# Kernel optimization log

Measured on AMD Instinct MI355X. Metric: run time of the kernel, lower is better.

The kernel has to match this reference:

```python
import jax, jax.numpy as jnp
import numpy as np

DIM = 1024
HEADS = 16
HEAD_DIM = DIM // HEADS
SCALE = HEAD_DIM ** -0.5


def setup_inputs() -> dict:
    key = jax.random.key(0)
    ks = jax.random.split(key, 6)
    B, N, C = 2, 2048, DIM
    q = jax.random.normal(ks[0], (B, N, C), dtype=jnp.float32)
    k = jax.random.normal(ks[1], (B, N, C), dtype=jnp.float32)
    v = jax.random.normal(ks[2], (B, N, C), dtype=jnp.float32)
    # torch nn.Linear weights: out = x @ W.T (+ b); qkv has no bias (qkv_bias=False)
    W_qkv = jax.random.normal(ks[3], (3 * C, 3 * C), dtype=jnp.float32) * (3 * C) ** -0.5
    W_proj = jax.random.normal(ks[4], (C, C), dtype=jnp.float32) * C ** -0.5
    b_proj = jax.random.normal(ks[5], (C,), dtype=jnp.float32) * 0.02
    return {"q": q, "k": k, "v": v, "W_qkv": W_qkv, "W_proj": W_proj, "b_proj": b_proj}


def reference(q, k, v, W_qkv, W_proj, b_proj):
    B, N, C = q.shape
    # fused QKV projection on concatenated [q,k,v] -> [B,N,3C]
    qkv = jnp.concatenate([q, k, v], axis=-1) @ W_qkv.T
    qkv = qkv.reshape(B, N, 3, HEADS, HEAD_DIM).transpose(2, 0, 3, 1, 4)  # [3,B,H,N,hd]
    qh, kh, vh = qkv[0], qkv[1], qkv[2]
    attn = jnp.einsum('bhqd,bhkd->bhqk', qh, kh) * SCALE
    attn = jax.nn.softmax(attn, axis=-1)  # attn_drop is identity (p=0)
    x = jnp.einsum('bhqk,bhkd->bhqd', attn, vh)  # [B,H,N,hd]
    x = x.transpose(0, 2, 1, 3).reshape(B, N, C)
    x = x @ W_proj.T + b_proj  # proj_drop is identity (p=0)
    return x
```

## Files before the change

kernel.cpp:

```cpp
#include <hip/hip_runtime.h>
#include <hip/hip_bf16.h>
#include <stdint.h>

#define HEADS 16
#define HD 64
#define SEQ 2048
#define BATCH 2
#define CDIM 1024
#define MROWS (BATCH*SEQ)
#define K3C (3*CDIM)
#define QSCALE 0.1803368801111244f

typedef __bf16 bf16x8 __attribute__((ext_vector_type(8)));
typedef float  f32x4  __attribute__((ext_vector_type(4)));

__device__ __forceinline__ unsigned short f2bf(float f) {
    __hip_bfloat16 h = __float2bfloat16(f);
    return __builtin_bit_cast(unsigned short, h);
}
__device__ __forceinline__ unsigned int pack2bf(float a, float b) {
    return (unsigned int)f2bf(a) | ((unsigned int)f2bf(b) << 16);
}
__device__ __forceinline__ bf16x8 frag(uint4 u) { return __builtin_bit_cast(bf16x8, u); }

__device__ __forceinline__ void async16(const unsigned short* g, unsigned short* lds) {
    __builtin_amdgcn_global_load_lds(
        (const __attribute__((address_space(1))) unsigned int*)g,
        (__attribute__((address_space(3))) unsigned int*)lds, 16, 0, 0);
}

__global__ void cast_all(const float* __restrict__ q, const float* __restrict__ k,
                         const float* __restrict__ v, const float* __restrict__ Wq,
                         const float* __restrict__ Wp,
                         unsigned short* __restrict__ A, unsigned short* __restrict__ Wqb,
                         unsigned short* __restrict__ Wpb)
{
    const int bid = blockIdx.x;
    const int t = threadIdx.x;
    if (bid < MROWS) {
        const float* srcs[3] = {q, k, v};
        #pragma unroll
        for (int i = 0; i < 3; ++i) {
            float4 f = *(const float4*)(srcs[i] + (size_t)bid*CDIM + t*4);
            ushort4 s;
            s.x = f2bf(f.x); s.y = f2bf(f.y); s.z = f2bf(f.z); s.w = f2bf(f.w);
            *(ushort4*)(A + (size_t)bid*K3C + i*CDIM + t*4) = s;
        }
    } else if (bid < MROWS + 9216) {
        int idx = (bid - MROWS)*256 + t;
        float4 f = ((const float4*)Wq)[idx];
        ushort4 s;
        s.x = f2bf(f.x); s.y = f2bf(f.y); s.z = f2bf(f.z); s.w = f2bf(f.w);
        ((ushort4*)Wqb)[idx] = s;
    } else {
        int idx = (bid - MROWS - 9216)*256 + t;
        float4 f = ((const float4*)Wp)[idx];
        ushort4 s;
        s.x = f2bf(f.x); s.y = f2bf(f.y); s.z = f2bf(f.z); s.w = f2bf(f.w);
        ((ushort4*)Wpb)[idx] = s;
    }
}

template<int EPI>
__global__ __launch_bounds__(256, 2)
void gemm_bt(const unsigned short* __restrict__ A, const unsigned short* __restrict__ B,
             int M, int N, int K,
             unsigned short* __restrict__ qh, unsigned short* __restrict__ kh,
             unsigned short* __restrict__ vt,
             const float* __restrict__ bias, float* __restrict__ out)
{
    __shared__ __attribute__((aligned(16))) unsigned short As[128*32];
    __shared__ __attribute__((aligned(16))) unsigned short Bs[128*32];
    const int tid  = threadIdx.x;
    const int wave = tid >> 6;
    const int lane = tid & 63;
    const int l15  = lane & 15;
    const int quad = lane >> 4;
    const int wm = (wave >> 1) * 64;
    const int wn = (wave & 1) * 64;
    const int m0 = blockIdx.x * 128;
    const int n0 = blockIdx.y * 128;

    f32x4 acc[4][4] = {};

    const int srow = tid >> 2;
    const int sc8  = (tid & 3) * 8;

    for (int k0 = 0; k0 < K; k0 += 32) {
        #pragma unroll
        for (int t = 0; t < 2; ++t) {
            int row = t*64 + srow;
            const unsigned short* ga = A + (size_t)(m0 + row)*K + k0 + sc8;
            const unsigned short* gb = B + (size_t)(n0 + row)*K + k0 + sc8;
            async16(ga, &As[(t*256 + wave*64)*8]);
            async16(gb, &Bs[(t*256 + wave*64)*8]);
        }
        __syncthreads();
        uint4 af[4], bfv[4];
        #pragma unroll
        for (int i = 0; i < 4; ++i) {
            af[i]  = *(const uint4*)&As[(wm + i*16 + l15)*32 + quad*8];
            bfv[i] = *(const uint4*)&Bs[(wn + i*16 + l15)*32 + quad*8];
        }
        #pragma unroll
        for (int mi = 0; mi < 4; ++mi)
            #pragma unroll
            for (int ni = 0; ni < 4; ++ni)
                acc[mi][ni] = __builtin_amdgcn_mfma_f32_16x16x32_bf16(
                    frag(af[mi]), frag(bfv[ni]), acc[mi][ni], 0, 0, 0);
        __syncthreads();
    }

    if constexpr (EPI == 0) {
        #pragma unroll
        for (int mi = 0; mi < 4; ++mi) {
            int row0 = m0 + wm + mi*16 + quad*4;
            int b  = row0 >> 11;
            int nq = row0 & 2047;
            #pragma unroll
            for (int ni = 0; ni < 4; ++ni) {
                int col   = n0 + wn + ni*16 + l15;
                int which = col >> 10;
                int h     = (col >> 6) & 15;
                int d     = col & 63;
                int bh    = b*HEADS + h;
                if (which == 2) {
                    ushort4 pv;
                    pv.x = f2bf(acc[mi][ni][0]);
                    pv.y = f2bf(acc[mi][ni][1]);
                    pv.z = f2bf(acc[mi][ni][2]);
                    pv.w = f2bf(acc[mi][ni][3]);
                    *(ushort4*)&vt[((size_t)bh*HD + d)*SEQ + nq] = pv;
                } else {
                    unsigned short* dst = (which == 0) ? qh : kh;
                    float sc = (which == 0) ? QSCALE : 1.0f;
                    #pragma unroll
                    for (int r = 0; r < 4; ++r)
                        dst[((size_t)bh*SEQ + nq + r)*HD + d] = f2bf(acc[mi][ni][r] * sc);
                }
            }
        }
    } else {
        #pragma unroll
        for (int mi = 0; mi < 4; ++mi) {
            int row0 = m0 + wm + mi*16 + quad*4;
            #pragma unroll
            for (int ni = 0; ni < 4; ++ni) {
                int col  = n0 + wn + ni*16 + l15;
                float bv = bias[col];
                #pragma unroll
                for (int r = 0; r < 4; ++r)
                    out[(size_t)(row0 + r)*N + col] = acc[mi][ni][r] + bv;
            }
        }
    }
}

__global__ __launch_bounds__(256, 2)
void attention(const unsigned short* __restrict__ qh, const unsigned short* __restrict__ kh,
               const unsigned short* __restrict__ vt, unsigned short* __restrict__ xb)
{
    const int qt = blockIdx.x;
    const int h  = blockIdx.y;
    const int b  = blockIdx.z;
    const int bh = b*HEADS + h;
    const int tid  = threadIdx.x;
    const int wave = tid >> 6;
    const int lane = tid & 63;
    const int l15  = lane & 15;
    const int quad = lane >> 4;

    __shared__ __attribute__((aligned(16))) unsigned short Ks[2][64*64];
    __shared__ __attribute__((aligned(16))) unsigned short Vs[2][64*64];
    __shared__ __attribute__((aligned(16))) unsigned short Ps[4][2*16*72];

    const unsigned short* Qp = qh + ((size_t)bh*SEQ + qt*128 + wave*32)*HD;
    const unsigned short* Kp = kh + (size_t)bh*SEQ*HD;
    const unsigned short* Vp = vt + (size_t)bh*HD*SEQ;

    auto stage = [&](int kt, int bufI) {
        #pragma unroll
        for (int t = 0; t < 2; ++t) {
            int c  = t*256 + wave*64 + lane;
            int r  = c >> 3;
            int cc = (c & 7) ^ (r & 7);
            async16(Kp + (size_t)(kt*64 + r)*HD + cc*8,
                    &Ks[bufI][(t*256 + wave*64)*8]);
            async16(Vp + (size_t)r*SEQ + kt*64 + cc*8,
                    &Vs[bufI][(t*256 + wave*64)*8]);
        }
    };

    stage(0, 0);

    uint4 qf[2][2];
    #pragma unroll
    for (int g = 0; g < 2; ++g) {
        qf[g][0] = *(const uint4*)(Qp + (size_t)(g*16 + l15)*HD + quad*8);
        qf[g][1] = *(const uint4*)(Qp + (size_t)(g*16 + l15)*HD + 32 + quad*8);
    }

    f32x4 o[2][4] = {};
    float m_s[2] = {-INFINITY, -INFINITY};
    float l_s[2] = {0.f, 0.f};

    unsigned short* Pw = Ps[wave];
    const int x7 = l15 & 7;

    for (int kt = 0; kt < SEQ/64; ++kt) {
        stage((kt + 1) & 31, (kt + 1) & 1);
        asm volatile("s_waitcnt vmcnt(4)" ::: "memory");
        asm volatile("s_barrier" ::: "memory");

        const unsigned short* Kb = Ks[kt & 1];
        const unsigned short* Vb = Vs[kt & 1];

        f32x4 s[2][4];
        #pragma unroll
        for (int st = 0; st < 4; ++st) {
            int rb = st*16 + l15;
            uint4 kf0 = *(const uint4*)&Kb[(rb*8 + (quad ^ x7))*8];
            uint4 kf1 = *(const uint4*)&Kb[(rb*8 + ((4 + quad) ^ x7))*8];
            #pragma unroll
            for (int g = 0; g < 2; ++g) {
                f32x4 z = {};
                z = __builtin_amdgcn_mfma_f32_16x16x32_bf16(frag(kf0), frag(qf[g][0]), z, 0, 0, 0);
                z = __builtin_amdgcn_mfma_f32_16x16x32_bf16(frag(kf1), frag(qf[g][1]), z, 0, 0, 0);
                s[g][st] = z;
            }
        }

        #pragma unroll
        for (int g = 0; g < 2; ++g) {
            float mloc = s[g][0][0];
            #pragma unroll
            for (int st = 0; st < 4; ++st)
                #pragma unroll
                for (int r = 0; r < 4; ++r)
                    mloc = fmaxf(mloc, s[g][st][r]);
            mloc = fmaxf(mloc, __shfl_xor(mloc, 16));
            mloc = fmaxf(mloc, __shfl_xor(mloc, 32));

            float mn = fmaxf(m_s[g], mloc);
            float al = __builtin_amdgcn_exp2f(m_s[g] - mn);
            m_s[g] = mn;

            float rs = 0.f;
            float p[4][4];
            #pragma unroll
            for (int st = 0; st < 4; ++st)
                #pragma unroll
                for (int r = 0; r < 4; ++r) {
                    p[st][r] = __builtin_amdgcn_exp2f(s[g][st][r] - mn);
                    rs += p[st][r];
                }
            rs += __shfl_xor(rs, 16);
            rs += __shfl_xor(rs, 32);
            l_s[g] = al*l_s[g] + rs;

            #pragma unroll
            for (int st = 0; st < 4; ++st)
                #pragma unroll
                for (int r = 0; r < 4; ++r)
                    o[g][st][r] *= al;

            #pragma unroll
            for (int st = 0; st < 4; ++st) {
                uint2 pk;
                pk.x = pack2bf(p[st][0], p[st][1]);
                pk.y = pack2bf(p[st][2], p[st][3]);
                *(uint2*)&Pw[g*1152 + l15*72 + st*16 + quad*4] = pk;
            }
        }
        asm volatile("s_waitcnt lgkmcnt(0)" ::: "memory");

        uint4 pB[2][2];
        #pragma unroll
        for (int g = 0; g < 2; ++g) {
            pB[g][0] = *(const uint4*)&Pw[g*1152 + l15*72 + quad*8];
            pB[g][1] = *(const uint4*)&Pw[g*1152 + l15*72 + 32 + quad*8];
        }

        #pragma unroll
        for (int st = 0; st < 4; ++st) {
            int rb = st*16 + l15;
            uint4 vf0 = *(const uint4*)&Vb[(rb*8 + (quad ^ x7))*8];
            uint4 vf1 = *(const uint4*)&Vb[(rb*8 + ((4 + quad) ^ x7))*8];
            #pragma unroll
            for (int g = 0; g < 2; ++g) {
                o[g][st] = __builtin_amdgcn_mfma_f32_16x16x32_bf16(frag(vf0), frag(pB[g][0]), o[g][st], 0, 0, 0);
                o[g][st] = __builtin_amdgcn_mfma_f32_16x16x32_bf16(frag(vf1), frag(pB[g][1]), o[g][st], 0, 0, 0);
            }
        }

        asm volatile("s_barrier" ::: "memory");
    }

    #pragma unroll
    for (int g = 0; g < 2; ++g) {
        float inv = 1.0f / l_s[g];
        #pragma unroll
        for (int st = 0; st < 4; ++st) {
            uint2 pk;
            pk.x = pack2bf(o[g][st][0]*inv, o[g][st][1]*inv);
            pk.y = pack2bf(o[g][st][2]*inv, o[g][st][3]*inv);
            *(uint2*)&Pw[g*1152 + l15*72 + st*16 + quad*4] = pk;
        }
    }
    asm volatile("s_waitcnt lgkmcnt(0)" ::: "memory");

    const int qr = lane >> 2;
    const int dd = (lane & 3) * 16;
    #pragma unroll
    for (int g = 0; g < 2; ++g) {
        uint4 oa = *(const uint4*)&Pw[g*1152 + qr*72 + dd];
        uint4 ob = *(const uint4*)&Pw[g*1152 + qr*72 + dd + 8];
        const int mrow = b*SEQ + qt*128 + wave*32 + g*16 + qr;
        *(uint4*)&xb[(size_t)mrow*CDIM + h*HD + dd]     = oa;
        *(uint4*)&xb[(size_t)mrow*CDIM + h*HD + dd + 8] = ob;
    }
}

extern "C" void kernel_launch(void* const* d_in, const int* in_sizes, int n_in,
                              void* d_out, int out_size, void* d_ws, size_t ws_size,
                              hipStream_t stream)
{
    const float* q  = (const float*)d_in[0];
    const float* k  = (const float*)d_in[1];
    const float* v  = (const float*)d_in[2];
    const float* Wq = (const float*)d_in[3];
    const float* Wp = (const float*)d_in[4];
    const float* bp = (const float*)d_in[5];
    float* out = (float*)d_out;

    char* p = (char*)d_ws;
    auto carve = [&](size_t bytes) { char* r = p; p += (bytes + 255) & ~(size_t)255; return r; };
    unsigned short* Abuf   = (unsigned short*)carve((size_t)MROWS*K3C*2);
    unsigned short* Wqkvb  = (unsigned short*)carve((size_t)K3C*K3C*2);
    unsigned short* Wprojb = (unsigned short*)carve((size_t)CDIM*CDIM*2);
    unsigned short* qhb    = (unsigned short*)carve((size_t)BATCH*HEADS*SEQ*HD*2);
    unsigned short* khb    = (unsigned short*)carve((size_t)BATCH*HEADS*SEQ*HD*2);
    unsigned short* vtb    = (unsigned short*)carve((size_t)BATCH*HEADS*SEQ*HD*2);
    unsigned short* xbuf   = (unsigned short*)carve((size_t)MROWS*CDIM*2);

    cast_all<<<MROWS + 9216 + 1024, 256, 0, stream>>>(q, k, v, Wq, Wp, Abuf, Wqkvb, Wprojb);

    gemm_bt<0><<<dim3(MROWS/128, K3C/128), 256, 0, stream>>>(
        Abuf, Wqkvb, MROWS, K3C, K3C, qhb, khb, vtb, nullptr, nullptr);

    attention<<<dim3(SEQ/128, HEADS, BATCH), 256, 0, stream>>>(qhb, khb, vtb, xbuf);

    gemm_bt<1><<<dim3(MROWS/128, CDIM/128), 256, 0, stream>>>(
        xbuf, Wprojb, MROWS, CDIM, CDIM, nullptr, nullptr, nullptr, bp, out);
}
```

Measured before the change: 301.3 us.

## Add 256x256-tile pipelined QKV GEMM kernel with 8 waves

Replaces the 128x128-tile QKV projection GEMM with a dedicated 256x256-tile kernel using 512 threads, double-buffered async global-to-LDS loads, swizzled LDS layout, and a four-phase interleaving of LDS reads, async stages and MFMA blocks with priority hints. A block-id swizzle groups tiles for L2 reuse. Larger tiles raise arithmetic intensity and the explicit schedule aims to hide load latency behind MFMA. The cost is a grid of only 192 blocks, which is below one block per CU on a 256-CU part, plus heavy register pressure and a fragile hand-tuned waitcnt schedule.

Result: no change. 305.2 us (+1.3%).

```diff
diff --git a/kernel.cpp b/kernel.cpp
--- a/kernel.cpp
+++ b/kernel.cpp
@@ -156,6 +156,185 @@
     }
 }
 
+#define NT48 48
+
+__global__ __launch_bounds__(512, 2)
+void gemm256_qkv(const unsigned short* __restrict__ A, const unsigned short* __restrict__ B,
+                 unsigned short* __restrict__ qh, unsigned short* __restrict__ kh,
+                 unsigned short* __restrict__ vt)
+{
+    __shared__ __attribute__((aligned(16))) unsigned short As[2*16384];
+    __shared__ __attribute__((aligned(16))) unsigned short Bs[2*16384];
+
+    const int tid  = threadIdx.x;
+    const int wave = tid >> 6;
+    const int lane = tid & 63;
+    const int l15  = lane & 15;
+    const int quad = lane >> 4;
+    const int wr   = wave >> 2;
+    const int wc   = wave & 3;
+
+    const int id  = blockIdx.x;
+    const int swz = (id & 7)*24 + (id >> 3);
+    const int m0  = (swz & 15) * 256;
+    const int n0  = (swz >> 4) * 256;
+
+    int lrr[2], kel[2];
+    #pragma unroll
+    for (int j = 0; j < 2; ++j) {
+        int p  = (j*512 + tid) * 16;
+        int st = p >> 10;
+        int q  = p & 1023;
+        int ql = q ^ (((q >> 9) & 1) << 5);
+        lrr[j] = (st >> 1)*16 + (ql >> 6);
+        kel[j] = (st & 1)*32 + ((ql & 63) >> 1);
+    }
+    const int ldsc = wave*64*8;
+
+    auto stageA = [&](int t, int g) {
+        unsigned short* dst = As + (t & 1)*16384 + g*8192;
+        #pragma unroll
+        for (int j = 0; j < 2; ++j) {
+            int grow = (lrr[j] >> 6)*128 + g*64 + (lrr[j] & 63);
+            async16(A + (size_t)(m0 + grow)*K3C + t*64 + kel[j], dst + j*4096 + ldsc);
+        }
+    };
+    auto stageB = [&](int t, int g) {
+        unsigned short* dst = Bs + (t & 1)*16384 + g*8192;
+        #pragma unroll
+        for (int j = 0; j < 2; ++j) {
+            int grow = (lrr[j] >> 5)*64 + g*32 + (lrr[j] & 31);
+            async16(B + (size_t)(n0 + grow)*K3C + t*64 + kel[j], dst + j*4096 + ldsc);
+        }
+    };
+
+    const int laneoff = (((l15*64 + quad*16) ^ ((l15 & 8) << 2)) >> 1);
+
+    f32x4 acc[8][4] = {};
+
+    stageA(0, 0); stageB(0, 0); stageA(0, 1); stageB(0, 1);
+    stageA(1, 0); stageB(1, 0); stageA(1, 1);
+    asm volatile("s_waitcnt vmcnt(6)" ::: "memory");
+    __builtin_amdgcn_s_barrier();
+
+    for (int tt = 0; tt < NT48; tt += 2) {
+        #pragma unroll
+        for (int hb = 0; hb < 2; ++hb) {
+            const int t = tt + hb;
+            const unsigned short* Ab = As + hb*16384 + laneoff;
+            const unsigned short* Bb = Bs + hb*16384 + laneoff;
+            uint4 ar[4][2], bl[2][2], bh[2][2];
+
+            #pragma unroll
+            for (int mi = 0; mi < 4; ++mi)
+                #pragma unroll
+                for (int kc = 0; kc < 2; ++kc)
+                    ar[mi][kc] = *(const uint4*)&Ab[((wr*4 + mi)*2 + kc)*512];
+            #pragma unroll
+            for (int ni = 0; ni < 2; ++ni)
+                #pragma unroll
+                for (int kc = 0; kc < 2; ++kc)
+                    bl[ni][kc] = *(const uint4*)&Bb[((wc*2 + ni)*2 + kc)*512];
+            if (t + 1 < NT48) stageB(t + 1, 1);
+            __builtin_amdgcn_s_barrier();
+            __builtin_amdgcn_s_setprio(1);
+            #pragma unroll
+            for (int mi = 0; mi < 4; ++mi)
+                #pragma unroll
+                for (int ni = 0; ni < 2; ++ni)
+                    #pragma unroll
+                    for (int kc = 0; kc < 2; ++kc)
+                        acc[mi][ni] = __builtin_amdgcn_mfma_f32_16x16x32_bf16(
+                            frag(ar[mi][kc]), frag(bl[ni][kc]), acc[mi][ni], 0, 0, 0);
+            __builtin_amdgcn_s_setprio(0);
+            __builtin_amdgcn_s_barrier();
+
+            #pragma unroll
+            for (int ni = 0; ni < 2; ++ni)
+                #pragma unroll
+                for (int kc = 0; kc < 2; ++kc)
+                    bh[ni][kc] = *(const uint4*)&Bb[8192 + ((wc*2 + ni)*2 + kc)*512];
+            if (t + 2 < NT48) stageA(t + 2, 0);
+            __builtin_amdgcn_s_barrier();
+            __builtin_amdgcn_s_setprio(1);
+            #pragma unroll
+            for (int mi = 0; mi < 4; ++mi)
+                #pragma unroll
+                for (int ni = 0; ni < 2; ++ni)
+                    #pragma unroll
+                    for (int kc = 0; kc < 2; ++kc)
+                        acc[mi][ni+2] = __builtin_amdgcn_mfma_f32_16x16x32_bf16(
+                            frag(ar[mi][kc]), frag(bh[ni][kc]), acc[mi][ni+2], 0, 0, 0);
+            __builtin_amdgcn_s_setprio(0);
+            __builtin_amdgcn_s_barrier();
+
+            #pragma unroll
+            for (int mi = 0; mi < 4; ++mi)
+                #pragma unroll
+                for (int kc = 0; kc < 2; ++kc)
+                    ar[mi][kc] = *(const uint4*)&Ab[8192 + ((wr*4 + mi)*2 + kc)*512];
+            if (t + 2 < NT48) stageB(t + 2, 0);
+            __builtin_amdgcn_s_barrier();
+            __builtin_amdgcn_s_setprio(1);
+            #pragma unroll
+            for (int mi = 0; mi < 4; ++mi)
+                #pragma unroll
+                for (int ni = 0; ni < 2; ++ni)
+                    #pragma unroll
+                    for (int kc = 0; kc < 2; ++kc)
+                        acc[mi+4][ni] = __builtin_amdgcn_mfma_f32_16x16x32_bf16(
+                            frag(ar[mi][kc]), frag(bl[ni][kc]), acc[mi+4][ni], 0, 0, 0);
+            __builtin_amdgcn_s_setprio(0);
+            __builtin_amdgcn_s_barrier();
+
+            if (t + 2 < NT48) stageA(t + 2, 1);
+            if (t + 2 < NT48)      { asm volatile("s_waitcnt vmcnt(6)" ::: "memory"); }
+            else if (t + 1 < NT48) { asm volatile("s_waitcnt vmcnt(0)" ::: "memory"); }
+            __builtin_amdgcn_s_barrier();
+            __builtin_amdgcn_s_setprio(1);
+            #pragma unroll
+            for (int mi = 0; mi < 4; ++mi)
+                #pragma unroll
+                for (int ni = 0; ni < 2; ++ni)
+                    #pragma unroll
+                    for (int kc = 0; kc < 2; ++kc)
+                        acc[mi+4][ni+2] = __builtin_amdgcn_mfma_f32_16x16x32_bf16(
+                            frag(ar[mi][kc]), frag(bh[ni][kc]), acc[mi+4][ni+2], 0, 0, 0);
+            __builtin_amdgcn_s_setprio(0);
+            __builtin_amdgcn_s_barrier();
+        }
+    }
+
+    #pragma unroll
+    for (int mi = 0; mi < 8; ++mi) {
+        const int row0 = m0 + wr*128 + mi*16 + quad*4;
+        const int b  = row0 >> 11;
+        const int nq = row0 & 2047;
+        #pragma unroll
+        for (int ni = 0; ni < 4; ++ni) {
+            const int col   = n0 + wc*64 + ni*16 + l15;
+            const int which = col >> 10;
+            const int h     = (col >> 6) & 15;
+            const int d     = col & 63;
+            const int bh_   = b*HEADS + h;
+            if (which == 2) {
+                ushort4 pv;
+                pv.x = f2bf(acc[mi][ni][0]);
+                pv.y = f2bf(acc[mi][ni][1]);
+                pv.z = f2bf(acc[mi][ni][2]);
+                pv.w = f2bf(acc[mi][ni][3]);
+                *(ushort4*)&vt[((size_t)bh_*HD + d)*SEQ + nq] = pv;
+            } else {
+                unsigned short* dst = (which == 0) ? qh : kh;
+                float sc = (which == 0) ? QSCALE : 1.0f;
+                #pragma unroll
+                for (int r = 0; r < 4; ++r)
+                    dst[((size_t)bh_*SEQ + nq + r)*HD + d] = f2bf(acc[mi][ni][r] * sc);
+            }
+        }
+    }
+}
+
 __global__ __launch_bounds__(256, 2)
 void attention(const unsigned short* __restrict__ qh, const unsigned short* __restrict__ kh,
                const unsigned short* __restrict__ vt, unsigned short* __restrict__ xb)
@@ -345,8 +524,7 @@
 
     cast_all<<<MROWS + 9216 + 1024, 256, 0, stream>>>(q, k, v, Wq, Wp, Abuf, Wqkvb, Wprojb);
 
-    gemm_bt<0><<<dim3(MROWS/128, K3C/128), 256, 0, stream>>>(
-        Abuf, Wqkvb, MROWS, K3C, K3C, qhb, khb, vtb, nullptr, nullptr);
+    gemm256_qkv<<<dim3(192), 512, 0, stream>>>(Abuf, Wqkvb, qhb, khb, vtb);
 
     attention<<<dim3(SEQ/128, HEADS, BATCH), 256, 0, stream>>>(qhb, khb, vtb, xbuf);
 
```
